# Kernel optimization log

Measured on AMD Instinct MI355X. Metric: run time of the kernel, lower is better.

## Reference

```python
import jax, jax.numpy as jnp
import numpy as np

MODE1 = 12
MODE2 = 12
WIDTH = 64
L = 10
DEPTH = 4
PAD = 9
EPS = 1e-5


def conv1x1(x, w, b):
    # x: (B,Ci,H,W), w: (Co,Ci), b: (Co,)
    return jnp.einsum('oi,bihw->bohw', w, x) + b[None, :, None, None]


def group_norm(x, gamma, beta, groups=2):
    B, C, H, W = x.shape
    xg = x.reshape(B, groups, C // groups, H, W)
    mu = xg.mean(axis=(2, 3, 4), keepdims=True)
    var = xg.var(axis=(2, 3, 4), keepdims=True)
    xn = ((xg - mu) * jax.lax.rsqrt(var + EPS)).reshape(B, C, H, W)
    return xn * gamma[None, :, None, None] + beta[None, :, None, None]


def spectral_conv(x, w1, w2):
    # x: (B,Ci,H,W); w1,w2: (Ci,Co,m1,m2,2) real/imag stacked
    B, Ci, H, W = x.shape
    Co = w1.shape[1]
    x_ft = jnp.fft.rfft2(x)  # (B,Ci,H,W//2+1) complex
    w1c = w1[..., 0] + 1j * w1[..., 1]
    w2c = w2[..., 0] + 1j * w2[..., 1]
    t1 = jnp.einsum('bixy,ioxy->boxy', x_ft[:, :, :MODE1, :MODE2], w1c)
    t2 = jnp.einsum('bixy,ioxy->boxy', x_ft[:, :, -MODE1:, :MODE2], w2c)
    out_ft = jnp.zeros((B, Co, H, W // 2 + 1), dtype=x_ft.dtype)
    out_ft = out_ft.at[:, :, :MODE1, :MODE2].set(t1)
    out_ft = out_ft.at[:, :, -MODE1:, :MODE2].set(t2)
    return jnp.fft.irfft2(out_ft, s=(H, W))


def mlp_block(x, w1, b1, g, bt, w2, b2):
    x = conv1x1(x, w1, b1)
    x = group_norm(x, g, bt)
    x = jax.nn.gelu(x, approximate=False)
    return conv1x1(x, w2, b2)


def get_grid(B, S):
    gx = jnp.linspace(0.0, 1.0, S, dtype=jnp.float32)
    gy = jnp.linspace(0.0, 1.0, S, dtype=jnp.float32)
    gridx = jnp.broadcast_to(gx[None, :, None, None], (B, S, S, 1))
    gridy = jnp.broadcast_to(gy[None, None, :, None], (B, S, S, 1))
    return jnp.concatenate([gridx, gridy], axis=-1)  # (B,S,S,2)


def pos_encoding(grid):
    # grid: (B,S,S,2) -> (B,S,S,4L); cos over all L then sin over all L,
    # within each L the 2 grid channels stay adjacent (matches torch cat order)
    freqs = (jnp.pi * (2.0 ** jnp.arange(L))).astype(jnp.float32)  # (L,)
    phase = grid[..., None, :] * freqs[:, None]  # (B,S,S,L,2)
    B, S1, S2 = grid.shape[:3]
    phase = phase.reshape(B, S1, S2, L * 2)
    return jnp.concatenate([jnp.cos(phase), jnp.sin(phase)], axis=-1)


def setup_inputs() -> dict:
    key = jax.random.key(0)
    ks = jax.random.split(key, 24)
    B, S = 8, 192
    Cin = 3 + 4 * L  # 43
    Wd = WIDTH
    scale = 1.0 / (Wd * Wd)
    d = {}
    d['x'] = jax.random.normal(ks[0], (B, S, S, 1), dtype=jnp.float32)
    d['Wp'] = jax.random.normal(ks[1], (Cin, Wd), dtype=jnp.float32) / np.sqrt(Cin)
    d['bp'] = jnp.zeros((Wd,), dtype=jnp.float32)
    d['sw1'] = scale * jax.random.uniform(ks[2], (DEPTH, Wd, Wd, MODE1, MODE2, 2), dtype=jnp.float32)
    d['sw2'] = scale * jax.random.uniform(ks[3], (DEPTH, Wd, Wd, MODE1, MODE2, 2), dtype=jnp.float32)
    d['m1w'] = jax.random.normal(ks[4], (DEPTH, Wd, Wd), dtype=jnp.float32) / np.sqrt(Wd)
    d['m1b'] = jnp.zeros((DEPTH, Wd), dtype=jnp.float32)
    d['mg'] = jnp.ones((DEPTH, Wd), dtype=jnp.float32)
    d['mbt'] = jnp.zeros((DEPTH, Wd), dtype=jnp.float32)
    d['m2w'] = jax.random.normal(ks[5], (DEPTH, Wd, Wd), dtype=jnp.float32) / np.sqrt(Wd)
    d['m2b'] = jnp.zeros((DEPTH, Wd), dtype=jnp.float32)
    d['ww'] = jax.random.normal(ks[6], (DEPTH, Wd, Wd), dtype=jnp.float32) / np.sqrt(Wd)
    d['wb'] = jnp.zeros((DEPTH, Wd), dtype=jnp.float32)
    d['ng'] = jnp.ones((DEPTH, Wd), dtype=jnp.float32)
    d['nb'] = jnp.zeros((DEPTH, Wd), dtype=jnp.float32)
    Wq = Wd * 4
    d['q1w'] = jax.random.normal(ks[7], (Wq, Wd), dtype=jnp.float32) / np.sqrt(Wd)
    d['q1b'] = jnp.zeros((Wq,), dtype=jnp.float32)
    d['qg'] = jnp.ones((Wq,), dtype=jnp.float32)
    d['qbt'] = jnp.zeros((Wq,), dtype=jnp.float32)
    d['q2w'] = jax.random.normal(ks[8], (1, Wq), dtype=jnp.float32) / np.sqrt(Wq)
    d['q2b'] = jnp.zeros((1,), dtype=jnp.float32)
    return d


def reference(x, Wp, bp, sw1, sw2, m1w, m1b, mg, mbt, m2w, m2b, ww, wb, ng, nb,
              q1w, q1b, qg, qbt, q2w, q2b):
    B, S = x.shape[0], x.shape[1]
    grid = get_grid(B, S)
    pe = pos_encoding(grid)
    h = jnp.concatenate([x, grid, pe], axis=-1)  # (B,S,S,43)
    h = h @ Wp + bp  # lift
    h = h.transpose(0, 3, 1, 2)  # (B,W,S,S)
    h = jnp.pad(h, ((0, 0), (0, 0), (0, PAD), (0, PAD)))
    for i in range(DEPTH):
        x1 = spectral_conv(h, sw1[i], sw2[i])
        x1 = mlp_block(x1, m1w[i], m1b[i], mg[i], mbt[i], m2w[i], m2b[i])
        x2 = conv1x1(h, ww[i], wb[i])
        x2 = group_norm(x2, ng[i], nb[i])
        h = x1 + x2
        if i != DEPTH - 1:
            h = jax.nn.gelu(h, approximate=False)
    h = h[..., :-PAD, :-PAD]
    h = mlp_block(h, q1w, q1b, qg, qbt, q2w, q2b)
    return h.transpose(0, 2, 3, 1)  # (B,S,S,1)
```

## Files before the change

### kernel.cpp

```cpp
#include <hip/hip_runtime.h>
#include <hip/hip_bf16.h>
#include <math.h>


#define NN 201
#define SS 192
#define NPIX 40401
#define QPIX 36864
#define BB 8
#define GNB 80
#define XWPL 1234944
#define PI_F 3.14159265358979323846f

typedef __hip_bfloat16 bf16;
typedef __attribute__((ext_vector_type(8))) short s8v;
typedef __attribute__((ext_vector_type(4))) float f32x4;

__device__ __forceinline__ float gelu_f(float x){
  float x2 = x*x;
  float t  = fmaf(x2, 0.0713548162f, 1.5957691216f);
  float e  = __expf(-x*t);
  return x*__builtin_amdgcn_rcpf(1.0f+e);
}
__device__ __forceinline__ float b2f(bf16 v){ return __bfloat162float(v); }
__device__ __forceinline__ bf16  f2b(float v){ return __float2bfloat16(v); }
__device__ __forceinline__ unsigned short f2bu(float x){
  bf16 h = __float2bfloat16(x);
  unsigned short u; __builtin_memcpy(&u,&h,2); return u;
}
__device__ __forceinline__ float bu2f(unsigned short u){
  unsigned int x = ((unsigned int)u)<<16; float f; __builtin_memcpy(&f,&x,4); return f;
}

__global__ void k_tab(float* __restrict__ tab){
  int t = blockIdx.x*blockDim.x+threadIdx.x;
  if(t>=13*NN) return;
  int k=t/NN, n=t-k*NN;
  int m=(k*n)%NN;
  float ang = (2.0f*PI_F/201.0f)*(float)m;
  tab[2*t]   = cosf(ang);
  tab[2*t+1] = sinf(ang);
}

__global__ void k_tpack(const float* __restrict__ tab, unsigned short* __restrict__ TPK){
  int e = blockIdx.x*256 + threadIdx.x;
  if(e>=6656) return;
  int wt=e>>9, lane=(e>>3)&63, j=e&7;
  int m_=lane&15, g=lane>>4;
  int w = wt*16+m_;
  int k24 = g*8+j;
  float v=0.f;
  if(k24<24 && w<201){
    float2 cs = ((const float2*)tab)[(k24>>1)*NN + w];
    v = (k24&1)? cs.y : cs.x;
  }
  TPK[e]=f2bu(v);
}

__global__ void k_tpack2(const float* __restrict__ tab, unsigned short* __restrict__ T2PK){
  int e = blockIdx.x*256 + threadIdx.x;
  if(e>=7168) return;
  int idx = e>>9;
  int mt = idx/7, chunk = idx - mt*7;
  int lane=(e>>3)&63, j=e&7;
  int m_=lane&15, g=lane>>4;
  int kx24 = mt*16 + m_;
  int w = chunk*32 + g*8 + j;
  float v=0.f;
  if(kx24<24 && w<NN){
    float2 cs = ((const float2*)tab)[(kx24>>1)*NN + w];
    v = (kx24&1)? -cs.y : cs.x;
  }
  T2PK[e]=f2bu(v);
}

__global__ void k_pretab(const float* __restrict__ Wp, const float* __restrict__ bp,
                         float* __restrict__ Ux, float* __restrict__ Uy){
  int i = blockIdx.x;
  int ax = blockIdx.y;
  int c = threadIdx.x;
  float g = (float)i*(1.0f/191.0f);
  float acc;
  if(ax==0) acc = bp[c] + g*Wp[64+c];
  else      acc = g*Wp[128+c];
  int cosBase = (ax==0)? 3 : 4;
  int sinBase = (ax==0)? 23 : 24;
  #pragma unroll
  for(int l=0;l<10;l++){
    float f = PI_F*(float)(1<<l);
    float sv,cv;
    sincosf(g*f,&sv,&cv);
    acc += cv*Wp[(cosBase+2*l)*64+c] + sv*Wp[(sinBase+2*l)*64+c];
  }
  float* U = (ax==0)? Ux : Uy;
  U[i*64+c] = acc;
}

__global__ void k_wpack(const float* __restrict__ m1w, const float* __restrict__ m2w,
                        const float* __restrict__ ww,  const float* __restrict__ q1w,
                        unsigned short* __restrict__ WPK){
  int bx = blockIdx.x, tid = threadIdx.x;
  const float* src;
  if(bx<12){
    int l=bx/3, sel=bx-l*3;
    src = (sel==0)? m1w+(size_t)l*4096 : (sel==1)? m2w+(size_t)l*4096 : ww+(size_t)l*4096;
  } else {
    src = q1w + (size_t)(bx-12)*4096;
  }
  unsigned short* dst = WPK + (size_t)bx*4096;
  #pragma unroll
  for(int t=0;t<16;t++){
    int d = tid*16+t;
    int frag=d>>9, lane=(d>>3)&63, j=d&7;
    int mt=frag>>1, kh=frag&1, m_=lane&15, g=lane>>4;
    dst[d] = f2bu(src[(size_t)(16*mt+m_)*64 + 32*kh + 8*g + j]);
  }
}

__global__ void __launch_bounds__(256) k_wtrans(const float* __restrict__ w1,
        const float* __restrict__ w2, float* __restrict__ WT){
  __shared__ float tile[64][65];
  int io0 = blockIdx.x*64;
  int c0  = blockIdx.y*64;
  int z   = blockIdx.z;
  const float* src = (z==0)? w1 : w2;
  int tid = threadIdx.x;
  #pragma unroll
  for(int it=0;it<16;it++){
    int e = tid + 256*it;
    int r = e>>6, c = e&63;
    if(c0+c<288) tile[r][c] = src[(size_t)(io0+r)*288 + c0 + c];
  }
  __syncthreads();
  #pragma unroll
  for(int it=0;it<16;it++){
    int e = tid + 256*it;
    int rp = e>>6, cp = e&63;
    int col = c0 + rp;
    if(col<288){
      int ky = col/24, rm = col - ky*24;
      int kx = rm>>1, comp = rm&1;
      int m = z*144 + ky*12 + kx;
      WT[(size_t)m*8192 + comp*4096 + io0 + cp] = tile[cp][rp];
    }
  }
}

__global__ void k_encoder(const float* __restrict__ x, const float* __restrict__ Wp,
                          const float* __restrict__ Ux, const float* __restrict__ Uy,
                          bf16* __restrict__ A){
  int tid=threadIdx.x;
  int p = blockIdx.x*256+tid;
  if(p>=NPIX) return;
  int b = blockIdx.y;
  uint4* dst = (uint4*)(A + ((size_t)b*NPIX + p)*64);
  int hh=p/NN, ww=p-hh*NN;
  if(hh>=SS || ww>=SS){
    uint4 z = {0,0,0,0};
    #pragma unroll
    for(int i=0;i<8;i++) dst[i]=z;
    return;
  }
  float xv = x[((size_t)b*SS+hh)*SS+ww];
  const float4* ux = (const float4*)(Ux + hh*64);
  const float4* uy = (const float4*)(Uy + ww*64);
  const float4* w0 = (const float4*)Wp;
  #pragma unroll
  for(int i=0;i<8;i++){
    float4 a0 = ux[2*i],   a1 = ux[2*i+1];
    float4 b0 = uy[2*i],   b1 = uy[2*i+1];
    float4 c0 = w0[2*i],   c1 = w0[2*i+1];
    float v0=xv*c0.x+a0.x+b0.x, v1=xv*c0.y+a0.y+b0.y;
    float v2=xv*c0.z+a0.z+b0.z, v3=xv*c0.w+a0.w+b0.w;
    float v4=xv*c1.x+a1.x+b1.x, v5=xv*c1.y+a1.y+b1.y;
    float v6=xv*c1.z+a1.z+b1.z, v7=xv*c1.w+a1.w+b1.w;
    uint4 v;
    v.x = (unsigned)f2bu(v0) | ((unsigned)f2bu(v1)<<16);
    v.y = (unsigned)f2bu(v2) | ((unsigned)f2bu(v3)<<16);
    v.z = (unsigned)f2bu(v4) | ((unsigned)f2bu(v5)<<16);
    v.w = (unsigned)f2bu(v6) | ((unsigned)f2bu(v7)<<16);
    dst[i]=v;
  }
}

__global__ void __launch_bounds__(256) k_dftw(const bf16* __restrict__ A,
        const unsigned short* __restrict__ T2PK, float* __restrict__ XW){
  int tid=threadIdx.x, wid=tid>>6, l=tid&63;
  int m_=l&15, g=l>>4;
  int R = blockIdx.x*4 + wid;
  const bf16* row = A + (size_t)R*NN*64;
  f32x4 acc[2][4];
  #pragma unroll
  for(int mt=0;mt<2;mt++){
    #pragma unroll
    for(int nt=0;nt<4;nt++) acc[mt][nt]=f32x4{0.f,0.f,0.f,0.f};
  }
  for(int chunk=0;chunk<7;chunk++){
    int wbase = chunk*32 + g*8;
    s8v bf[4];
    if(chunk<6){
      #pragma unroll
      for(int nt=0;nt<4;nt++){
        s8v f;
        #pragma unroll
        for(int j=0;j<8;j++){
          unsigned short v;
          bf16 hv = row[(size_t)(wbase+j)*64 + 16*nt + m_];
          __builtin_memcpy(&v,&hv,2);
          f[j]=(short)v;
        }
        bf[nt]=f;
      }
    } else {
      #pragma unroll
      for(int nt=0;nt<4;nt++){
        s8v f;
        #pragma unroll
        for(int j=0;j<8;j++){
          unsigned short v=0;
          if(wbase+j<NN){
            bf16 hv = row[(size_t)(wbase+j)*64 + 16*nt + m_];
            __builtin_memcpy(&v,&hv,2);
          }
          f[j]=(short)v;
        }
        bf[nt]=f;
      }
    }
    #pragma unroll
    for(int mt=0;mt<2;mt++){
      s8v af = *(const s8v*)(T2PK + (size_t)(mt*7+chunk)*512 + l*8);
      #pragma unroll
      for(int nt=0;nt<4;nt++)
        acc[mt][nt]=__builtin_amdgcn_mfma_f32_16x16x32_bf16(af,bf[nt],acc[mt][nt],0,0,0);
    }
  }
  #pragma unroll
  for(int mt=0;mt<2;mt++){
    #pragma unroll
    for(int nt=0;nt<4;nt++){
      #pragma unroll
      for(int e=0;e<4;e++){
        int kx24 = mt*16 + 4*g + e;
        if(kx24<24){
          int plane = kx24&1, kx = kx24>>1;
          XW[(size_t)plane*XWPL + ((size_t)R*12+kx)*64 + 16*nt + m_] = acc[mt][nt][e];
        }
      }
    }
  }
}

__global__ void __launch_bounds__(256) k_dfth(const float* __restrict__ XW,
        const float* __restrict__ tab, float* __restrict__ XF){
  __shared__ float sre[201*32];
  __shared__ float sim[201*32];
  __shared__ float2 tw[13*NN];
  int kx=blockIdx.x, b=blockIdx.y;
  int z=blockIdx.z; int jh=z>>1, ch=z&1;
  int tid=threadIdx.x;
  for(int i=tid;i<13*NN;i+=256) tw[i]=((const float2*)tab)[i];
  for(int i=tid;i<201*32;i+=256){
    int h=i>>5, c=ch*32+(i&31);
    size_t idx=(((size_t)b*NN+h)*12+kx)*64+c;
    sre[i]=XW[idx];
    sim[i]=XW[idx+XWPL];
  }
  __syncthreads();
  for(int o=tid;o<384;o+=256){
    int jj=o>>5, cl=o&31;
    int j=jh*12+jj;
    int k2=(j<12)?j:24-j;
    float sgn=(j<12)?-1.f:1.f;
    float re0=0.f,im0=0.f,re1=0.f,im1=0.f;
    const float* pr=sre+cl;
    const float* pi=sim+cl;
    const float2* tk=tw+k2*NN;
    int h=0;
    for(;h+1<NN;h+=2){
      float a0=pr[h*32], b0=pi[h*32];
      float2 cs0=tk[h];
      float c0=cs0.x, s0=sgn*cs0.y;
      re0 = fmaf(a0,c0, fmaf(-b0,s0, re0));
      im0 = fmaf(a0,s0, fmaf( b0,c0, im0));
      float a1=pr[(h+1)*32], b1=pi[(h+1)*32];
      float2 cs1=tk[h+1];
      float c1=cs1.x, s1=sgn*cs1.y;
      re1 = fmaf(a1,c1, fmaf(-b1,s1, re1));
      im1 = fmaf(a1,s1, fmaf( b1,c1, im1));
    }
    {
      float a0=pr[h*32], b0=pi[h*32];
      float2 cs0=tk[h];
      float c0=cs0.x, s0=sgn*cs0.y;
      re0 = fmaf(a0,c0, fmaf(-b0,s0, re0));
      im0 = fmaf(a0,s0, fmaf( b0,c0, im0));
    }
    int m=j*12+kx;
    int c=ch*32+cl;
    XF[(size_t)m*1024+(b*64+c)*2]  =re0+re1;
    XF[(size_t)m*1024+(b*64+c)*2+1]=im0+im1;
  }
}

__global__ void __launch_bounds__(512) k_modemix(const float* __restrict__ XF,
     const float* __restrict__ WT, float* __restrict__ XO){
  __shared__ float sx[1024];
  __shared__ float swr[4096], swi[4096];
  int m=blockIdx.x;
  int tid=threadIdx.x;
  sx[tid]     = XF[(size_t)m*1024+tid];
  sx[tid+512] = XF[(size_t)m*1024+tid+512];
  const float* wr = WT + (size_t)m*8192;
  const float* wi = wr + 4096;
  for(int io=tid;io<4096;io+=512){
    swr[io]=wr[io];
    swi[io]=wi[io];
  }
  __syncthreads();
  int b=tid>>6, o=tid&63;
  const float* xb = sx + b*128;
  float re0=0.f,re1=0.f,im0=0.f,im1=0.f;
  #pragma unroll 8
  for(int i=0;i<64;i+=2){
    float a=xb[2*i], b2=xb[2*i+1];
    float c=swr[i*64+o], d=swi[i*64+o];
    re0 = fmaf(a,c, fmaf(-b2,d, re0));
    im0 = fmaf(a,d, fmaf( b2,c, im0));
    float a1=xb[2*i+2], b3=xb[2*i+3];
    float c1=swr[(i+1)*64+o], d1=swi[(i+1)*64+o];
    re1 = fmaf(a1,c1, fmaf(-b3,d1, re1));
    im1 = fmaf(a1,d1, fmaf( b3,c1, im1));
  }
  XO[2*((size_t)m*512+tid)]  =re0+re1;
  XO[2*((size_t)m*512+tid)+1]=im0+im1;
}

__global__ void __launch_bounds__(256) k_ispec(const float* __restrict__ XO,
        const float* __restrict__ tab, const unsigned short* __restrict__ TPK,
        bf16* __restrict__ C){
  __shared__ float2 yl[12][64];
  __shared__ float2 cs13[13];
  int R=blockIdx.x;
  int b=R/NN, h=R-b*NN;
  int tid=threadIdx.x;
  if(tid<13) cs13[tid]=((const float2*)tab)[tid*NN+h];
  __syncthreads();
  const float sc = 1.0f/40401.0f;
  #pragma unroll
  for(int it=0;it<3;it++){
    int item = tid + 256*it;
    int kx = item>>6, o = item&63;
    float re0=0.f,im0=0.f,re1=0.f,im1=0.f;
    #pragma unroll
    for(int j=0;j<24;j+=2){
      {
        int k2=(j<12)?j:24-j;
        float sgn=(j<12)?1.0f:-1.0f;
        float2 xo = *(const float2*)(XO + 2*(((size_t)(j*12+kx)*512) + b*64 + o));
        float2 cs = cs13[k2];
        float cc=cs.x, s2=sgn*cs.y;
        re0 = fmaf(xo.x,cc, fmaf(-xo.y,s2, re0));
        im0 = fmaf(xo.x,s2, fmaf( xo.y,cc, im0));
      }
      {
        int j1=j+1;
        int k2=(j1<12)?j1:24-j1;
        float sgn=(j1<12)?1.0f:-1.0f;
        float2 xo = *(const float2*)(XO + 2*(((size_t)(j1*12+kx)*512) + b*64 + o));
        float2 cs = cs13[k2];
        float cc=cs.x, s2=sgn*cs.y;
        re1 = fmaf(xo.x,cc, fmaf(-xo.y,s2, re1));
        im1 = fmaf(xo.x,s2, fmaf( xo.y,cc, im1));
      }
    }
    float fr = (kx==0)? sc : 2.0f*sc;
    float fi = (kx==0)? sc : -2.0f*sc;
    yl[kx][o] = float2{ (re0+re1)*fr, (im0+im1)*fi };
  }
  __syncthreads();
  int wid=tid>>6, l=tid&63, m_=l&15, g=l>>4;
  int o = wid*16 + m_;
  s8v bfr;
  #pragma unroll
  for(int j=0;j<4;j++){
    float2 v = yl[4*g+j][o];
    bfr[2*j]   = (short)f2bu(v.x);
    bfr[2*j+1] = (short)f2bu(v.y);
  }
  bf16* cp = C + (size_t)R*NN*64;
  #pragma unroll
  for(int wt=0; wt<13; wt++){
    s8v af = *(const s8v*)(TPK + (size_t)wt*512 + l*8);
    f32x4 acc = f32x4{0.f,0.f,0.f,0.f};
    acc = __builtin_amdgcn_mfma_f32_16x16x32_bf16(af, bfr, acc, 0,0,0);
    #pragma unroll
    for(int e=0;e<4;e++){
      int w = wt*16 + 4*g + e;
      if(w<NN) cp[(size_t)w*64 + o] = f2b(acc[e]);
    }
  }
}

__global__ void __launch_bounds__(256) k_gramC(const float* __restrict__ XO,
        float* __restrict__ GCp, float* __restrict__ SC){
  __shared__ unsigned short V[64][72];
  int chunk=blockIdx.x, b=blockIdx.y, tid=threadIdx.x;
  const float s1=1.0f/201.0f;
  const float r2=0.70710678118f;
  const float q2=1.41421356237f;
  #pragma unroll
  for(int it=0;it<16;it++){
    int e = tid + it*256;
    int fl=e>>6, ch=e&63;
    int f = chunk*64 + fl;
    int base = b*64+ch;
    float v=0.f;
    if(f<528){
      int comp=f&1, kxm=f>>1;
      int kx0=kxm/24;
      int kx=1+kx0, m=kxm-kx0*24;
      v = q2*XO[2*((size_t)(m*12+kx)*512 + base)+comp];
    } else if(f==528){
      v = XO[2*(size_t)base];
    } else if(f<551){
      int q=f-529; int mm=1+(q>>1);
      const float* p1 = XO + 2*((size_t)(mm*12)*512 + base);
      const float* p2 = XO + 2*((size_t)((24-mm)*12)*512 + base);
      v = ((q&1)==0)? r2*(p1[0]+p2[0]) : r2*(p1[1]-p2[1]);
    } else if(f==551){
      v = r2*XO[2*((size_t)(144)*512 + base)];
    } else if(f==552){
      v = r2*XO[2*((size_t)(144)*512 + base)+1];
    }
    V[ch][fl]=f2bu(v*s1);
  }
  __syncthreads();
  int wid=tid>>6, l=tid&63, m_=l&15, g=l>>4;
  f32x4 acc[4];
  #pragma unroll
  for(int mt=0;mt<4;mt++) acc[mt]=f32x4{0.f,0.f,0.f,0.f};
  #pragma unroll
  for(int kc=0;kc<2;kc++){
    s8v bfr = *(const s8v*)&V[16*wid+m_][kc*32+8*g];
    #pragma unroll
    for(int mt=0;mt<4;mt++){
      s8v afr = *(const s8v*)&V[16*mt+m_][kc*32+8*g];
      acc[mt]=__builtin_amdgcn_mfma_f32_16x16x32_bf16(afr,bfr,acc[mt],0,0,0);
    }
  }
  float* gb = GCp + ((size_t)(b*9+chunk))*4096;
  #pragma unroll
  for(int mt=0;mt<4;mt++){
    #pragma unroll
    for(int e=0;e<4;e++)
      gb[(size_t)(16*mt+4*g+e)*64 + 16*wid + m_] = acc[mt][e];
  }
  if(chunk==0 && tid<64) SC[b*64+tid] = XO[2*(size_t)(b*64+tid)];
}

__global__ void k_gcred(const float* __restrict__ GCp, float* __restrict__ GC){
  int b=blockIdx.y;
  int idx=blockIdx.x*256+threadIdx.x;
  float s=0.f;
  #pragma unroll
  for(int k=0;k<9;k++) s += GCp[((size_t)(b*9+k))*4096 + idx];
  GC[(size_t)b*4096 + idx]=s;
}

__global__ void __launch_bounds__(256) k_gramp(const bf16* __restrict__ X,
        float* __restrict__ Gpart, float* __restrict__ Spart, int HR, int WR){
  int b = blockIdx.y, blk = blockIdx.x;
  int npix = HR*WR;
  int tid=threadIdx.x, wid=tid>>6, l=tid&63;
  int m_=l&15, g=l>>4;
  int slab = blk*4 + wid;
  const bf16* xb = X + (size_t)b*NPIX*64;
  f32x4 acc[4][4];
  #pragma unroll
  for(int mt=0;mt<4;mt++){
    #pragma unroll
    for(int nt=0;nt<4;nt++) acc[mt][nt]=f32x4{0.f,0.f,0.f,0.f};
  }
  float cs[4]={0.f,0.f,0.f,0.f};
  for(int kc=0;kc<16;kc++){
    int pbase = slab*512 + kc*32 + g*8;
    int hh0=0, ww0=0;
    if(WR!=NN){ hh0 = pbase/WR; ww0 = pbase - hh0*WR; }
    const bf16* ptr[8];
    #pragma unroll
    for(int jj=0;jj<8;jj++){
      int p = pbase + jj;
      int gp;
      if(WR==NN) gp = p;
      else {
        int ww2 = ww0 + jj;
        int hh  = hh0;
        if(ww2>=WR){ ww2-=WR; hh++; }
        gp = hh*NN + ww2;
      }
      ptr[jj] = (p<npix) ? (xb + (size_t)gp*64) : (const bf16*)0;
    }
    s8v fr[4];
    #pragma unroll
    for(int t=0;t<4;t++){
      s8v f;
      float s=0.f;
      #pragma unroll
      for(int jj=0;jj<8;jj++){
        unsigned short v=0;
        if(ptr[jj]){ bf16 hv = ptr[jj][16*t+m_]; __builtin_memcpy(&v,&hv,2); }
        f[jj]=(short)v;
        s += bu2f(v);
      }
      fr[t]=f;
      cs[t]+=s;
    }
    #pragma unroll
    for(int nt=0;nt<4;nt++){
      #pragma unroll
      for(int mt=0;mt<4;mt++)
        acc[mt][nt]=__builtin_amdgcn_mfma_f32_16x16x32_bf16(fr[mt],fr[nt],acc[mt][nt],0,0,0);
    }
  }
  float* gp_ = Gpart + ((size_t)(b*GNB + slab))*4096;
  #pragma unroll
  for(int mt=0;mt<4;mt++){
    #pragma unroll
    for(int nt=0;nt<4;nt++){
      #pragma unroll
      for(int e=0;e<4;e++)
        gp_[(size_t)(16*mt + 4*g + e)*64 + 16*nt + m_] = acc[mt][nt][e];
    }
  }
  #pragma unroll
  for(int t=0;t<4;t++){
    float s=cs[t];
    s += __shfl_xor(s,16,64);
    s += __shfl_xor(s,32,64);
    if(g==0) Spart[((size_t)(b*GNB+slab))*64 + 16*t + m_] = s;
  }
}

__global__ void __launch_bounds__(256) k_gramr(const float* __restrict__ Gpart,
        const float* __restrict__ Spart, float* __restrict__ Gfin,
        float* __restrict__ Sfin, int nblk){
  int b = blockIdx.y;
  int idx = blockIdx.x*256 + threadIdx.x;
  float s0=0.f,s1=0.f,s2=0.f,s3=0.f;
  int k=0;
  for(;k+3<nblk;k+=4){
    s0 += Gpart[((size_t)b*GNB + k  )*4096 + idx];
    s1 += Gpart[((size_t)b*GNB + k+1)*4096 + idx];
    s2 += Gpart[((size_t)b*GNB + k+2)*4096 + idx];
    s3 += Gpart[((size_t)b*GNB + k+3)*4096 + idx];
  }
  for(;k<nblk;k++) s0 += Gpart[((size_t)b*GNB + k)*4096 + idx];
  Gfin[(size_t)b*4096 + idx] = (s0+s1)+(s2+s3);
  if(blockIdx.x==0 && threadIdx.x<64){
    float ss=0.f;
    for(int j=0;j<nblk;j++) ss += Spart[((size_t)b*GNB + j)*64 + threadIdx.x];
    Sfin[b*64 + threadIdx.x]=ss;
  }
}

__global__ void __launch_bounds__(256) k_statsA(
        const float* __restrict__ GC, const float* __restrict__ SC,
        const float* __restrict__ Gfin, const float* __restrict__ Sfin,
        const float* __restrict__ m1wl, const float* __restrict__ m1bl,
        const float* __restrict__ wwl,  const float* __restrict__ wbl,
        float* __restrict__ TSTAT, float* __restrict__ USTAT){
  __shared__ float Gs[4096];
  __shared__ float Ss[64];
  __shared__ float rs[256], rq[256];
  int zb2=blockIdx.x;
  int zb=zb2>>1, grp=zb2&1;
  int t=threadIdx.x;
  const float* GS  = (zb<8)? (GC + (size_t)zb*4096) : (Gfin + (size_t)(zb-8)*4096);
  const float* SS_ = (zb<8)? (SC + (size_t)zb*64)   : (Sfin + (size_t)(zb-8)*64);
  #pragma unroll
  for(int e=0;e<16;e++) Gs[t*16+e]=GS[t*16+e];
  if(t<64) Ss[t]=SS_[t];
  __syncthreads();
  const float* W    = (zb<8)? m1wl : wwl;
  const float* bias = (zb<8)? m1bl : wbl;
  float* stat       = (zb<8)? TSTAT : USTAT;
  int b = (zb<8)? zb : zb-8;
  int o = grp*32 + (t&31);
  int sl = t>>5;
  float w[64];
  #pragma unroll
  for(int j2=0;j2<64;j2++) w[j2]=bu2f(f2bu(W[(size_t)o*64+j2]));
  const float* Gr = Gs + (size_t)(sl*8)*64;
  float quad=0.f;
  #pragma unroll
  for(int r=0;r<8;r++){
    const float* gr = Gr + r*64;
    float tt=0.f;
    #pragma unroll
    for(int j2=0;j2<64;j2++) tt += gr[j2]*w[j2];
    quad += w[sl*8+r]*tt;
  }
  float sm=0.f, sq=quad;
  if(sl==0){
    float dot=0.f;
    #pragma unroll
    for(int j2=0;j2<64;j2++) dot += w[j2]*Ss[j2];
    float bo = bias[o];
    float Nf = (float)NPIX;
    sm = dot + Nf*bo;
    sq += 2.f*bo*dot + Nf*bo*bo;
  }
  rs[t]=sm; rq[t]=sq;
  __syncthreads();
  if(t<32){
    float s2=0.f,q2=0.f;
    #pragma unroll
    for(int k=0;k<8;k++){ s2+=rs[t+32*k]; q2+=rq[t+32*k]; }
    for(int off=16;off>0;off>>=1){
      s2 += __shfl_down(s2,off,32);
      q2 += __shfl_down(q2,off,32);
    }
    if(t==0){
      float invN = 1.f/((float)NPIX*32.f);
      float mean = s2*invN;
      float var = q2*invN - mean*mean;
      stat[b*4+grp*2]   = mean;
      stat[b*4+grp*2+1] = rsqrtf(fmaxf(var,0.f)+1e-5f);
    }
  }
}

__global__ void __launch_bounds__(256) k_statsQ(const float* __restrict__ Gfin,
        const float* __restrict__ Sfin,
        const float* __restrict__ W, const float* __restrict__ bias,
        float* __restrict__ QP){
  __shared__ float Gs[4096];
  __shared__ float Ss[64];
  __shared__ float rs[256], rq[256];
  int b=blockIdx.x, z=blockIdx.y, t=threadIdx.x;
  #pragma unroll
  for(int e=0;e<16;e++) Gs[t*16+e]=Gfin[(size_t)b*4096 + t*16+e];
  if(t<64) Ss[t]=Sfin[b*64+t];
  __syncthreads();
  int o = z*64 + (t&63);
  int sl = t>>6;
  float w[64];
  #pragma unroll
  for(int j2=0;j2<64;j2++) w[j2]=bu2f(f2bu(W[(size_t)o*64+j2]));
  const float* Gr = Gs + (size_t)(sl*16)*64;
  float quad=0.f;
  #pragma unroll
  for(int r=0;r<16;r++){
    const float* gr = Gr + r*64;
    float tt=0.f;
    #pragma unroll
    for(int j2=0;j2<64;j2++) tt += gr[j2]*w[j2];
    quad += w[sl*16+r]*tt;
  }
  float sm=0.f, sq=quad;
  if(sl==0){
    float dot=0.f;
    #pragma unroll
    for(int j2=0;j2<64;j2++) dot += w[j2]*Ss[j2];
    float bo=bias[o];
    float Nf=(float)QPIX;
    sm = dot + Nf*bo;
    sq += 2.f*bo*dot + Nf*bo*bo;
  }
  rs[t]=sm; rq[t]=sq;
  __syncthreads();
  if(t<64){
    float s2 = rs[t]+rs[t+64]+rs[t+128]+rs[t+192];
    float q2 = rq[t]+rq[t+64]+rq[t+128]+rq[t+192];
    for(int off=32;off>0;off>>=1){
      s2 += __shfl_down(s2,off,64);
      q2 += __shfl_down(q2,off,64);
    }
    if(t==0){
      int g = z>>1;
      atomicAdd(&QP[b*4+g*2],   s2);
      atomicAdd(&QP[b*4+g*2+1], q2);
    }
  }
}

__global__ void k_qfin(const float* __restrict__ QP, float* __restrict__ QSTAT){
  int t=threadIdx.x;
  if(t>=16) return;
  int b=t>>1, g=t&1;
  float s=QP[b*4+g*2], ss=QP[b*4+g*2+1];
  float invN=1.f/((float)QPIX*128.f);
  float mean=s*invN, var=ss*invN-mean*mean;
  QSTAT[b*4+g*2]   = mean;
  QSTAT[b*4+g*2+1] = rsqrtf(fmaxf(var,0.f)+1e-5f);
}

__global__ void __launch_bounds__(256) k_fuse(const bf16* __restrict__ Cb,
    bf16* __restrict__ A,
    const unsigned short* __restrict__ wp1, const float* __restrict__ m1b,
    const float* __restrict__ mg,  const float* __restrict__ mbt,
    const unsigned short* __restrict__ wp2, const float* __restrict__ m2b,
    const unsigned short* __restrict__ wpw, const float* __restrict__ wbk,
    const float* __restrict__ ng,  const float* __restrict__ nb,
    const float* __restrict__ tstat, const float* __restrict__ ustat, int last){
  __shared__ unsigned short vlds[4][64][72];
  int tid=threadIdx.x;
  int wid=tid>>6, l=tid&63;
  int m_=l&15, g=l>>4;
  int b=blockIdx.y;
  int p0=blockIdx.x*256 + wid*64;
  const bf16* cbb = Cb + (size_t)b*NPIX*64;
  const bf16* ab  = A  + (size_t)b*NPIX*64;

  s8v af[4][2];
  f32x4 acc[4][4];

  #pragma unroll
  for(int mt=0;mt<4;mt++){
    #pragma unroll
    for(int kh=0;kh<2;kh++)
      af[mt][kh]=*(const s8v*)(wp1 + (mt*2+kh)*512 + l*8);
    float4 b4 = *(const float4*)(m1b + 16*mt + 4*g);
    #pragma unroll
    for(int nt=0;nt<4;nt++) acc[mt][nt]=f32x4{b4.x,b4.y,b4.z,b4.w};
  }
  #pragma unroll
  for(int nt=0;nt<4;nt++){
    int p = p0 + 16*nt + m_;
    int pc = p<NPIX? p : NPIX-1;
    const s8v* xb = (const s8v*)(cbb + (size_t)pc*64);
    s8v b0 = xb[g], b1 = xb[4+g];
    #pragma unroll
    for(int mt=0;mt<4;mt++){
      acc[mt][nt]=__builtin_amdgcn_mfma_f32_16x16x32_bf16(af[mt][0],b0,acc[mt][nt],0,0,0);
      acc[mt][nt]=__builtin_amdgcn_mfma_f32_16x16x32_bf16(af[mt][1],b1,acc[mt][nt],0,0,0);
    }
  }
  {
    float tm0=tstat[b*4],tr0=tstat[b*4+1],tm1=tstat[b*4+2],tr1=tstat[b*4+3];
    #pragma unroll
    for(int mt=0;mt<4;mt++){
      float4 g4 = *(const float4*)(mg  + 16*mt + 4*g);
      float4 t4 = *(const float4*)(mbt + 16*mt + 4*g);
      float mn = (mt<2)? tm0 : tm1;
      float rs = (mt<2)? tr0 : tr1;
      float ax=rs*g4.x, ay=rs*g4.y, az=rs*g4.z, aw=rs*g4.w;
      float cx=t4.x-mn*ax, cy=t4.y-mn*ay, cz=t4.z-mn*az, cw=t4.w-mn*aw;
      #pragma unroll
      for(int nt=0;nt<4;nt++){
        int pl = 16*nt + m_;
        f32x4 t = acc[mt][nt];
        float v0 = gelu_f(fmaf(t[0],ax,cx));
        float v1 = gelu_f(fmaf(t[1],ay,cy));
        float v2 = gelu_f(fmaf(t[2],az,cz));
        float v3 = gelu_f(fmaf(t[3],aw,cw));
        uint2 pk;
        pk.x = (unsigned)f2bu(v0) | ((unsigned)f2bu(v1)<<16);
        pk.y = (unsigned)f2bu(v2) | ((unsigned)f2bu(v3)<<16);
        *(uint2*)&vlds[wid][pl][16*mt+4*g] = pk;
      }
    }
  }
  __syncthreads();
  #pragma unroll
  for(int mt=0;mt<4;mt++){
    #pragma unroll
    for(int kh=0;kh<2;kh++)
      af[mt][kh]=*(const s8v*)(wpw + (mt*2+kh)*512 + l*8);
    float4 b4 = *(const float4*)(wbk + 16*mt + 4*g);
    #pragma unroll
    for(int nt=0;nt<4;nt++) acc[mt][nt]=f32x4{b4.x,b4.y,b4.z,b4.w};
  }
  #pragma unroll
  for(int nt=0;nt<4;nt++){
    int p = p0 + 16*nt + m_;
    int pc = p<NPIX? p : NPIX-1;
    const s8v* xb = (const s8v*)(ab + (size_t)pc*64);
    s8v b0 = xb[g], b1 = xb[4+g];
    #pragma unroll
    for(int mt=0;mt<4;mt++){
      acc[mt][nt]=__builtin_amdgcn_mfma_f32_16x16x32_bf16(af[mt][0],b0,acc[mt][nt],0,0,0);
      acc[mt][nt]=__builtin_amdgcn_mfma_f32_16x16x32_bf16(af[mt][1],b1,acc[mt][nt],0,0,0);
    }
  }
  {
    float um0=ustat[b*4],ur0=ustat[b*4+1],um1=ustat[b*4+2],ur1=ustat[b*4+3];
    #pragma unroll
    for(int mt=0;mt<4;mt++){
      float4 n4 = *(const float4*)(ng  + 16*mt + 4*g);
      float4 nb4= *(const float4*)(nb  + 16*mt + 4*g);
      float4 m24= *(const float4*)(m2b + 16*mt + 4*g);
      float mn = (mt<2)? um0 : um1;
      float rs = (mt<2)? ur0 : ur1;
      float ax=rs*n4.x, ay=rs*n4.y, az=rs*n4.z, aw=rs*n4.w;
      float cx=m24.x+nb4.x-mn*ax, cy=m24.y+nb4.y-mn*ay;
      float cz=m24.z+nb4.z-mn*az, cw=m24.w+nb4.w-mn*aw;
      #pragma unroll
      for(int nt=0;nt<4;nt++){
        f32x4 u = acc[mt][nt];
        u[0] = fmaf(u[0],ax,cx);
        u[1] = fmaf(u[1],ay,cy);
        u[2] = fmaf(u[2],az,cz);
        u[3] = fmaf(u[3],aw,cw);
        acc[mt][nt]=u;
      }
    }
  }
  #pragma unroll
  for(int mt=0;mt<4;mt++){
    #pragma unroll
    for(int kh=0;kh<2;kh++)
      af[mt][kh]=*(const s8v*)(wp2 + (mt*2+kh)*512 + l*8);
  }
  #pragma unroll
  for(int nt=0;nt<4;nt++){
    int pl = 16*nt + m_;
    const s8v* vp = (const s8v*)&vlds[wid][pl][0];
    s8v b0 = vp[g], b1 = vp[4+g];
    #pragma unroll
    for(int mt=0;mt<4;mt++){
      acc[mt][nt]=__builtin_amdgcn_mfma_f32_16x16x32_bf16(af[mt][0],b0,acc[mt][nt],0,0,0);
      acc[mt][nt]=__builtin_amdgcn_mfma_f32_16x16x32_bf16(af[mt][1],b1,acc[mt][nt],0,0,0);
    }
  }
  #pragma unroll
  for(int nt=0;nt<4;nt++){
    int p = p0 + 16*nt + m_;
    if(p>=NPIX) continue;
    bf16* dp = A + ((size_t)b*NPIX + p)*64;
    #pragma unroll
    for(int mt=0;mt<4;mt++){
      f32x4 h = acc[mt][nt];
      float h0=h[0],h1=h[1],h2=h[2],h3=h[3];
      if(!last){ h0=gelu_f(h0); h1=gelu_f(h1); h2=gelu_f(h2); h3=gelu_f(h3); }
      uint2 pk;
      pk.x = (unsigned)f2bu(h0) | ((unsigned)f2bu(h1)<<16);
      pk.y = (unsigned)f2bu(h2) | ((unsigned)f2bu(h3)<<16);
      *(uint2*)(dp + 16*mt + 4*g) = pk;
    }
  }
}

__global__ void __launch_bounds__(256) k_qout(const bf16* __restrict__ A,
    const unsigned short* __restrict__ qpack, const float* __restrict__ q1b,
    const float* __restrict__ qg, const float* __restrict__ qbt,
    const float* __restrict__ q2w, const float* __restrict__ q2b,
    const float* __restrict__ qstat, float* __restrict__ out){
  __shared__ unsigned short xq[128][72];
  __shared__ float part[4][128];
  int tid=threadIdx.x;
  int wid=tid>>6, l=tid&63;
  int m_=l&15, g=l>>4;
  int b=blockIdx.y;
  int px0=blockIdx.x*128;
  {
    int p = px0 + (tid>>1);
    int half = tid&1;
    int hh=p/SS, ww2=p-hh*SS;
    const uint4* src=(const uint4*)(A + (((size_t)b*NPIX) + (size_t)hh*NN + ww2)*64 + half*32);
    uint4* drow=(uint4*)&xq[tid>>1][half*32];
    #pragma unroll
    for(int i=0;i<4;i++) drow[i]=src[i];
  }
  __syncthreads();
  int oc=wid;
  const unsigned short* wp = qpack + (size_t)oc*4096;
  s8v af[4][2];
  f32x4 bi4[4];
  float4 a4[4], c4[4], w4[4];
  float m0=qstat[b*4],r0=qstat[b*4+1],m1=qstat[b*4+2],r1=qstat[b*4+3];
  float mn=(oc<2)?m0:m1, rs=(oc<2)?r0:r1;
  #pragma unroll
  for(int mt=0;mt<4;mt++){
    #pragma unroll
    for(int kh=0;kh<2;kh++)
      af[mt][kh]=*(const s8v*)(wp + (mt*2+kh)*512 + l*8);
    float4 b4=*(const float4*)(q1b + 64*oc + 16*mt + 4*g);
    bi4[mt]=f32x4{b4.x,b4.y,b4.z,b4.w};
    float4 g4=*(const float4*)(qg  + 64*oc + 16*mt + 4*g);
    float4 t4=*(const float4*)(qbt + 64*oc + 16*mt + 4*g);
    w4[mt]=*(const float4*)(q2w + 64*oc + 16*mt + 4*g);
    a4[mt]=float4{rs*g4.x, rs*g4.y, rs*g4.z, rs*g4.w};
    c4[mt]=float4{t4.x-mn*a4[mt].x, t4.y-mn*a4[mt].y, t4.z-mn*a4[mt].z, t4.w-mn*a4[mt].w};
  }
  #pragma unroll
  for(int nt=0;nt<8;nt++){
    const s8v* vp = (const s8v*)&xq[16*nt+m_][0];
    s8v b0=vp[g], b1=vp[4+g];
    f32x4 acc[4];
    #pragma unroll
    for(int mt=0;mt<4;mt++) acc[mt]=bi4[mt];
    #pragma unroll
    for(int mt=0;mt<4;mt++){
      acc[mt]=__builtin_amdgcn_mfma_f32_16x16x32_bf16(af[mt][0],b0,acc[mt],0,0,0);
      acc[mt]=__builtin_amdgcn_mfma_f32_16x16x32_bf16(af[mt][1],b1,acc[mt],0,0,0);
    }
    float pp=0.f;
    #pragma unroll
    for(int mt=0;mt<4;mt++){
      f32x4 t=acc[mt];
      pp += gelu_f(fmaf(t[0],a4[mt].x,c4[mt].x))*w4[mt].x;
      pp += gelu_f(fmaf(t[1],a4[mt].y,c4[mt].y))*w4[mt].y;
      pp += gelu_f(fmaf(t[2],a4[mt].z,c4[mt].z))*w4[mt].z;
      pp += gelu_f(fmaf(t[3],a4[mt].w,c4[mt].w))*w4[mt].w;
    }
    pp += __shfl_xor(pp,16,64);
    pp += __shfl_xor(pp,32,64);
    if(g==0) part[wid][16*nt+m_]=pp;
  }
  __syncthreads();
  if(tid<128)
    out[(size_t)b*QPIX + px0 + tid] =
        q2b[0] + part[0][tid]+part[1][tid]+part[2][tid]+part[3][tid];
}

extern "C" void kernel_launch(void* const* d_in, const int* in_sizes, int n_in,
                              void* d_out, int out_size, void* d_ws, size_t ws_size,
                              hipStream_t stream){
  const float* x   = (const float*)d_in[0];
  const float* Wp  = (const float*)d_in[1];
  const float* bp  = (const float*)d_in[2];
  const float* sw1 = (const float*)d_in[3];
  const float* sw2 = (const float*)d_in[4];
  const float* m1w = (const float*)d_in[5];
  const float* m1b = (const float*)d_in[6];
  const float* mg  = (const float*)d_in[7];
  const float* mbt = (const float*)d_in[8];
  const float* m2w = (const float*)d_in[9];
  const float* m2b = (const float*)d_in[10];
  const float* ww  = (const float*)d_in[11];
  const float* wb  = (const float*)d_in[12];
  const float* ng  = (const float*)d_in[13];
  const float* nb  = (const float*)d_in[14];
  const float* q1w = (const float*)d_in[15];
  const float* q1b = (const float*)d_in[16];
  const float* qg  = (const float*)d_in[17];
  const float* qbt = (const float*)d_in[18];
  const float* q2w = (const float*)d_in[19];
  const float* q2b = (const float*)d_in[20];
  float* out = (float*)d_out;

  char* w8 = (char*)d_ws;
  const size_t ACT_B = (size_t)64*BB*NPIX*sizeof(bf16);
  bf16*  A    = (bf16*)(w8);
  bf16*  Cb   = (bf16*)(w8 + ACT_B);
  float* SPEC = (float*)(w8 + 2*ACT_B);
  float* XF   = (float*)(w8 + 2*ACT_B + 9879552);
  float* XO   = (float*)(w8 + 2*ACT_B + 9879552 + 1179648);
  float* TB   = (float*)(w8 + 2*ACT_B + 9879552 + 2*1179648);
  char*  g8   = w8 + 2*ACT_B + 9879552 + 2*1179648 + 20992;
  float* TSTAT= (float*)g8;
  float* USTAT= TSTAT + 32;
  float* QSTAT= USTAT + 32;
  float* UxT  = QSTAT + 32;
  float* UyT  = UxT + 12288;
  unsigned short* WPK = (unsigned short*)(UyT + 12288);
  float* GC   = (float*)(WPK + 16*4096);
  float* SC   = GC + 8*4096;
  float* GFIN = SC + 8*64;
  float* SFIN = GFIN + 8*4096;
  unsigned short* TPK = (unsigned short*)(SFIN + 8*64);
  unsigned short* T2PK = TPK + 6656;
  float* QP   = (float*)(T2PK + 7168);
  float* GCp  = SPEC;
  float* Gpart = SPEC;
  float* Spart = Gpart + (size_t)8*GNB*4096;
  float* WT = SPEC;
  size_t needed = (size_t)(2*ACT_B) + 9879552 + 2*1179648 + 20992
                + 3*32*4 + 2*12288*4 + 16*4096*2 + 2*(8*4096+8*64)*4
                + 13312 + 14336 + 128;
  if(ws_size < needed) return;

  k_tab<<<11,256,0,stream>>>(TB);
  k_tpack<<<26,256,0,stream>>>(TB, TPK);
  k_tpack2<<<28,256,0,stream>>>(TB, T2PK);
  k_pretab<<<dim3(192,2),64,0,stream>>>(Wp, bp, UxT, UyT);
  k_wpack<<<16,256,0,stream>>>(m1w, m2w, ww, q1w, WPK);
  k_encoder<<<dim3(158,BB),256,0,stream>>>(x, Wp, UxT, UyT, A);

  for(int l=0;l<4;l++){
    const float* sw1l = sw1 + (size_t)l*1179648;
    const float* sw2l = sw2 + (size_t)l*1179648;
    k_dftw<<<402,256,0,stream>>>(A, T2PK, SPEC);
    k_dfth<<<dim3(12,BB,4),256,0,stream>>>(SPEC, TB, XF);
    k_wtrans<<<dim3(64,5,2),256,0,stream>>>(sw1l, sw2l, WT);
    k_modemix<<<288,512,0,stream>>>(XF, WT, XO);
    k_ispec<<<1608,256,0,stream>>>(XO, TB, TPK, Cb);
    k_gramC<<<dim3(9,BB),256,0,stream>>>(XO, GCp, SC);
    k_gcred<<<dim3(16,BB),256,0,stream>>>(GCp, GC);
    k_gramp<<<dim3(20,BB),256,0,stream>>>(A, Gpart, Spart, NN, NN);
    k_gramr<<<dim3(16,BB),256,0,stream>>>(Gpart, Spart, GFIN, SFIN, 80);
    k_statsA<<<32,256,0,stream>>>(GC, SC, GFIN, SFIN,
          m1w + (size_t)l*4096, m1b + l*64, ww + (size_t)l*4096, wb + l*64,
          TSTAT, USTAT);
    k_fuse<<<dim3(158,BB),256,0,stream>>>(Cb, A,
          WPK + (size_t)(l*3+0)*4096, m1b + l*64, mg + l*64, mbt + l*64,
          WPK + (size_t)(l*3+1)*4096, m2b + l*64,
          WPK + (size_t)(l*3+2)*4096, wb  + l*64, ng + l*64, nb + l*64,
          TSTAT, USTAT, (l==3)?1:0);
  }

  k_gramp<<<dim3(18,BB),256,0,stream>>>(A, Gpart, Spart, SS, SS);
  k_gramr<<<dim3(16,BB),256,0,stream>>>(Gpart, Spart, GFIN, SFIN, 72);
  hipMemsetAsync(QP, 0, 32*sizeof(float), stream);
  k_statsQ<<<dim3(BB,4),256,0,stream>>>(GFIN, SFIN, q1w, q1b, QP);
  k_qfin<<<1,16,0,stream>>>(QP, QSTAT);
  k_qout<<<dim3(288,BB),256,0,stream>>>(A, WPK + (size_t)12*4096, q1b,
          qg, qbt, q2w, q2b, QSTAT, out);
}
```

Measured before the change: 858.2 us.

## Move H-axis DFT onto bf16 MFMA and fold Gram partial reduction into stats

The second (H-direction) DFT stage, previously a scalar FMA loop over shared memory, becomes an MFMA GEMM. It uses a new packed bf16 twiddle table that combines the real and imaginary planes into a K=402 contraction. The intermediate from the W-direction DFT is now stored as bf16 in a kx-major layout so the new kernel can read contiguous columns. The separate k_gcred reduction kernel is removed, and k_statsA sums the 9 partial Gram blocks directly, which saves one launch per layer. The intermediate spectrum now passes through bf16 twice, which lowers precision.

After: 837.7 us. 1.02x faster.

```diff
diff --git a/kernel.cpp b/kernel.cpp
--- a/kernel.cpp
+++ b/kernel.cpp
@@ -72,6 +72,29 @@
     v = (kx24&1)? -cs.y : cs.x;
   }
   T2PK[e]=f2bu(v);
+}
+
+__global__ void k_tpack3(const float* __restrict__ tab, unsigned short* __restrict__ T3PK){
+  int e = blockIdx.x*256 + threadIdx.x;
+  if(e>=19968) return;
+  int idx=e>>9;
+  int mt=idx/13, chunk=idx-mt*13;
+  int lane=(e>>3)&63, j=e&7;
+  int m_=lane&15, g=lane>>4;
+  int m = mt*16+m_;
+  int k = chunk*32+g*8+j;
+  float v=0.f;
+  if(m<48 && k<402){
+    int j24=m>>1, comp=m&1;
+    int k2=(j24<12)? j24 : 24-j24;
+    float sgn=(j24<12)? -1.f : 1.f;
+    int h=(k<201)? k : k-201;
+    float2 cs=((const float2*)tab)[k2*NN+h];
+    float cc=cs.x, ss=sgn*cs.y;
+    if(k<201) v = comp? ss : cc;
+    else      v = comp? cc : -ss;
+  }
+  T3PK[e]=f2bu(v);
 }
 
 __global__ void k_pretab(const float* __restrict__ Wp, const float* __restrict__ bp,
@@ -184,7 +207,7 @@
 }
 
 __global__ void __launch_bounds__(256) k_dftw(const bf16* __restrict__ A,
-        const unsigned short* __restrict__ T2PK, float* __restrict__ XW){
+        const unsigned short* __restrict__ T2PK, bf16* __restrict__ XWb){
   int tid=threadIdx.x, wid=tid>>6, l=tid&63;
   int m_=l&15, g=l>>4;
   int R = blockIdx.x*4 + wid;
@@ -235,6 +258,7 @@
         acc[mt][nt]=__builtin_amdgcn_mfma_f32_16x16x32_bf16(af,bf[nt],acc[mt][nt],0,0,0);
     }
   }
+  int bb = R/NN, h = R - bb*NN;
   #pragma unroll
   for(int mt=0;mt<2;mt++){
     #pragma unroll
@@ -244,62 +268,56 @@
         int kx24 = mt*16 + 4*g + e;
         if(kx24<24){
           int plane = kx24&1, kx = kx24>>1;
-          XW[(size_t)plane*XWPL + ((size_t)R*12+kx)*64 + 16*nt + m_] = acc[mt][nt][e];
+          XWb[(size_t)plane*XWPL + (((size_t)bb*12+kx)*201 + h)*64 + 16*nt + m_]
+            = f2b(acc[mt][nt][e]);
         }
       }
     }
   }
 }
 
-__global__ void __launch_bounds__(256) k_dfth(const float* __restrict__ XW,
-        const float* __restrict__ tab, float* __restrict__ XF){
-  __shared__ float sre[201*32];
-  __shared__ float sim[201*32];
-  __shared__ float2 tw[13*NN];
-  int kx=blockIdx.x, b=blockIdx.y;
-  int z=blockIdx.z; int jh=z>>1, ch=z&1;
-  int tid=threadIdx.x;
-  for(int i=tid;i<13*NN;i+=256) tw[i]=((const float2*)tab)[i];
-  for(int i=tid;i<201*32;i+=256){
-    int h=i>>5, c=ch*32+(i&31);
-    size_t idx=(((size_t)b*NN+h)*12+kx)*64+c;
-    sre[i]=XW[idx];
-    sim[i]=XW[idx+XWPL];
-  }
-  __syncthreads();
-  for(int o=tid;o<384;o+=256){
-    int jj=o>>5, cl=o&31;
-    int j=jh*12+jj;
-    int k2=(j<12)?j:24-j;
-    float sgn=(j<12)?-1.f:1.f;
-    float re0=0.f,im0=0.f,re1=0.f,im1=0.f;
-    const float* pr=sre+cl;
-    const float* pi=sim+cl;
-    const float2* tk=tw+k2*NN;
-    int h=0;
-    for(;h+1<NN;h+=2){
-      float a0=pr[h*32], b0=pi[h*32];
-      float2 cs0=tk[h];
-      float c0=cs0.x, s0=sgn*cs0.y;
-      re0 = fmaf(a0,c0, fmaf(-b0,s0, re0));
-      im0 = fmaf(a0,s0, fmaf( b0,c0, im0));
-      float a1=pr[(h+1)*32], b1=pi[(h+1)*32];
-      float2 cs1=tk[h+1];
-      float c1=cs1.x, s1=sgn*cs1.y;
-      re1 = fmaf(a1,c1, fmaf(-b1,s1, re1));
-      im1 = fmaf(a1,s1, fmaf( b1,c1, im1));
-    }
-    {
-      float a0=pr[h*32], b0=pi[h*32];
-      float2 cs0=tk[h];
-      float c0=cs0.x, s0=sgn*cs0.y;
-      re0 = fmaf(a0,c0, fmaf(-b0,s0, re0));
-      im0 = fmaf(a0,s0, fmaf( b0,c0, im0));
-    }
-    int m=j*12+kx;
-    int c=ch*32+cl;
-    XF[(size_t)m*1024+(b*64+c)*2]  =re0+re1;
-    XF[(size_t)m*1024+(b*64+c)*2+1]=im0+im1;
+__global__ void __launch_bounds__(256) k_dfthM(const bf16* __restrict__ XWb,
+        const unsigned short* __restrict__ T3PK, float* __restrict__ XF){
+  int kx=blockIdx.x, b=blockIdx.y, zh=blockIdx.z;
+  int tid=threadIdx.x, wid=tid>>6, l=tid&63;
+  int m_=l&15, g=l>>4;
+  if(wid>=3) return;
+  const bf16* base = XWb + (((size_t)b*12+kx)*201)*64;
+  f32x4 acc0=f32x4{0.f,0.f,0.f,0.f}, acc1=f32x4{0.f,0.f,0.f,0.f};
+  for(int chunk=0;chunk<13;chunk++){
+    s8v bf0, bf1;
+    #pragma unroll
+    for(int nt2=0;nt2<2;nt2++){
+      int c = 16*(zh*2+nt2) + m_;
+      s8v f;
+      #pragma unroll
+      for(int j=0;j<8;j++){
+        int k = chunk*32 + g*8 + j;
+        unsigned short v=0;
+        if(k<402){
+          int h = (k<201)? k : (k-201);
+          size_t poff = (k<201)? 0 : (size_t)XWPL;
+          bf16 hv = base[poff + (size_t)h*64 + c];
+          __builtin_memcpy(&v,&hv,2);
+        }
+        f[j]=(short)v;
+      }
+      if(nt2==0) bf0=f; else bf1=f;
+    }
+    s8v af = *(const s8v*)(T3PK + (size_t)(wid*13+chunk)*512 + l*8);
+    acc0=__builtin_amdgcn_mfma_f32_16x16x32_bf16(af,bf0,acc0,0,0,0);
+    acc1=__builtin_amdgcn_mfma_f32_16x16x32_bf16(af,bf1,acc1,0,0,0);
+  }
+  #pragma unroll
+  for(int nt2=0;nt2<2;nt2++){
+    f32x4 a = (nt2==0)? acc0 : acc1;
+    int c = 16*(zh*2+nt2) + m_;
+    #pragma unroll
+    for(int e2=0;e2<4;e2++){
+      int m = wid*16 + 4*g + e2;
+      int j24 = m>>1, comp = m&1;
+      XF[(size_t)(j24*12+kx)*1024 + ((size_t)b*64+c)*2 + comp] = a[e2];
+    }
   }
 }
 
@@ -459,15 +477,6 @@
   if(chunk==0 && tid<64) SC[b*64+tid] = XO[2*(size_t)(b*64+tid)];
 }
 
-__global__ void k_gcred(const float* __restrict__ GCp, float* __restrict__ GC){
-  int b=blockIdx.y;
-  int idx=blockIdx.x*256+threadIdx.x;
-  float s=0.f;
-  #pragma unroll
-  for(int k=0;k<9;k++) s += GCp[((size_t)(b*9+k))*4096 + idx];
-  GC[(size_t)b*4096 + idx]=s;
-}
-
 __global__ void __launch_bounds__(256) k_gramp(const bf16* __restrict__ X,
         float* __restrict__ Gpart, float* __restrict__ Spart, int HR, int WR){
   int b = blockIdx.y, blk = blockIdx.x;
@@ -565,7 +574,7 @@
 }
 
 __global__ void __launch_bounds__(256) k_statsA(
-        const float* __restrict__ GC, const float* __restrict__ SC,
+        const float* __restrict__ GCp, const float* __restrict__ SC,
         const float* __restrict__ Gfin, const float* __restrict__ Sfin,
         const float* __restrict__ m1wl, const float* __restrict__ m1bl,
         const float* __restrict__ wwl,  const float* __restrict__ wbl,
@@ -576,11 +585,21 @@
   int zb2=blockIdx.x;
   int zb=zb2>>1, grp=zb2&1;
   int t=threadIdx.x;
-  const float* GS  = (zb<8)? (GC + (size_t)zb*4096) : (Gfin + (size_t)(zb-8)*4096);
-  const float* SS_ = (zb<8)? (SC + (size_t)zb*64)   : (Sfin + (size_t)(zb-8)*64);
-  #pragma unroll
-  for(int e=0;e<16;e++) Gs[t*16+e]=GS[t*16+e];
-  if(t<64) Ss[t]=SS_[t];
+  if(zb<8){
+    #pragma unroll
+    for(int e=0;e<16;e++){
+      float s=0.f;
+      #pragma unroll
+      for(int q=0;q<9;q++) s += GCp[((size_t)(zb*9+q))*4096 + t*16+e];
+      Gs[t*16+e]=s;
+    }
+    if(t<64) Ss[t]=SC[zb*64+t];
+  } else {
+    const float* GS = Gfin + (size_t)(zb-8)*4096;
+    #pragma unroll
+    for(int e=0;e<16;e++) Gs[t*16+e]=GS[t*16+e];
+    if(t<64) Ss[t]=Sfin[(zb-8)*64+t];
+  }
   __syncthreads();
   const float* W    = (zb<8)? m1wl : wwl;
   const float* bias = (zb<8)? m1bl : wbl;
@@ -956,25 +975,27 @@
   float* UxT  = QSTAT + 32;
   float* UyT  = UxT + 12288;
   unsigned short* WPK = (unsigned short*)(UyT + 12288);
-  float* GC   = (float*)(WPK + 16*4096);
-  float* SC   = GC + 8*4096;
-  float* GFIN = SC + 8*64;
+  float* GFIN = (float*)(WPK + 16*4096);
   float* SFIN = GFIN + 8*4096;
-  unsigned short* TPK = (unsigned short*)(SFIN + 8*64);
+  float* SC   = SFIN + 8*64;
+  unsigned short* TPK = (unsigned short*)(SC + 8*64);
   unsigned short* T2PK = TPK + 6656;
-  float* QP   = (float*)(T2PK + 7168);
-  float* GCp  = SPEC;
+  unsigned short* T3PK = T2PK + 7168;
+  float* QP   = (float*)(T3PK + 19968);
+  float* GCp  = QP + 32;
+  bf16*  XWb  = (bf16*)SPEC;
   float* Gpart = SPEC;
   float* Spart = Gpart + (size_t)8*GNB*4096;
   float* WT = SPEC;
   size_t needed = (size_t)(2*ACT_B) + 9879552 + 2*1179648 + 20992
-                + 3*32*4 + 2*12288*4 + 16*4096*2 + 2*(8*4096+8*64)*4
-                + 13312 + 14336 + 128;
+                + 3*32*4 + 2*12288*4 + 16*4096*2 + (8*4096+2*8*64)*4
+                + 13312 + 14336 + 39936 + 128 + (size_t)8*9*4096*4;
   if(ws_size < needed) return;
 
   k_tab<<<11,256,0,stream>>>(TB);
   k_tpack<<<26,256,0,stream>>>(TB, TPK);
   k_tpack2<<<28,256,0,stream>>>(TB, T2PK);
+  k_tpack3<<<78,256,0,stream>>>(TB, T3PK);
   k_pretab<<<dim3(192,2),64,0,stream>>>(Wp, bp, UxT, UyT);
   k_wpack<<<16,256,0,stream>>>(m1w, m2w, ww, q1w, WPK);
   k_encoder<<<dim3(158,BB),256,0,stream>>>(x, Wp, UxT, UyT, A);
@@ -982,16 +1003,15 @@
   for(int l=0;l<4;l++){
     const float* sw1l = sw1 + (size_t)l*1179648;
     const float* sw2l = sw2 + (size_t)l*1179648;
-    k_dftw<<<402,256,0,stream>>>(A, T2PK, SPEC);
-    k_dfth<<<dim3(12,BB,4),256,0,stream>>>(SPEC, TB, XF);
+    k_dftw<<<402,256,0,stream>>>(A, T2PK, XWb);
+    k_dfthM<<<dim3(12,BB,2),256,0,stream>>>(XWb, T3PK, XF);
     k_wtrans<<<dim3(64,5,2),256,0,stream>>>(sw1l, sw2l, WT);
     k_modemix<<<288,512,0,stream>>>(XF, WT, XO);
     k_ispec<<<1608,256,0,stream>>>(XO, TB, TPK, Cb);
     k_gramC<<<dim3(9,BB),256,0,stream>>>(XO, GCp, SC);
-    k_gcred<<<dim3(16,BB),256,0,stream>>>(GCp, GC);
     k_gramp<<<dim3(20,BB),256,0,stream>>>(A, Gpart, Spart, NN, NN);
     k_gramr<<<dim3(16,BB),256,0,stream>>>(Gpart, Spart, GFIN, SFIN, 80);
-    k_statsA<<<32,256,0,stream>>>(GC, SC, GFIN, SFIN,
+    k_statsA<<<32,256,0,stream>>>(GCp, SC, GFIN, SFIN,
           m1w + (size_t)l*4096, m1b + l*64, ww + (size_t)l*4096, wb + l*64,
           TSTAT, USTAT);
     k_fuse<<<dim3(158,BB),256,0,stream>>>(Cb, A,
```
